# Optimization experiments

Measured on AMD Instinct MI355X. Metric: run time of the kernel, lower is better.

Reference implementation:

```python
import jax, jax.numpy as jnp
import numpy as np

N = 65536    # collocation points
N1 = 1024    # RBF centers
EPS = 0.1    # multiscale parameter used for width init scale


def setup_inputs() -> dict:
    key = jax.random.key(0)
    ks = jax.random.split(key, 10)
    x = jax.random.uniform(ks[0], (N, 2), dtype=jnp.float32)

    def mk(i):
        h = jax.random.uniform(ks[3 * i + 1], (N1,), dtype=jnp.float32)
        c = jax.random.uniform(ks[3 * i + 2], (N1, 2), dtype=jnp.float32)
        w = 5.0 * jax.random.uniform(ks[3 * i + 3], (N1, 2), dtype=jnp.float32) / EPS
        return h, c, w

    h1, c1, w1 = mk(0)
    h2, c2, w2 = mk(1)
    h3, c3, w3 = mk(2)
    return dict(x=x, hight=h1, center=c1, width=w1,
                hight2=h2, center2=c2, width2=w2,
                hight3=h3, center3=c3, width3=w3)


def _rbf(X, c, h, w):
    """Gaussian RBF expansion. X:(N,2) points, c:(N1,2) centers,
    h:(N1,) heights, w:(N1,2) widths. Returns u, du/dx, du/dy, each (N,)."""
    x1 = X[:, 0:1] - c[None, :, 0]          # (N, N1)
    y1 = X[:, 1:2] - c[None, :, 1]          # (N, N1)
    d1 = w[:, 0] ** 2                        # (N1,)
    d2 = w[:, 1] ** 2                        # (N1,)
    e = jnp.exp(-(x1 ** 2) * d1 - (y1 ** 2) * d2)  # (N, N1)
    u = e @ h                                # (N,)
    ux = (-2.0 * x1 * d1 * e) @ h            # (N,)
    uy = (-2.0 * y1 * d2 * e) @ h            # (N,)
    return u, ux, uy


def reference(x, hight, center, width, hight2, center2, width2,
              hight3, center3, width3):
    _, ux, uy = _rbf(x, center, hight, width)
    P, Px, _ = _rbf(x, center2, hight2, width2)
    Q, _, Qy = _rbf(x, center3, hight3, width3)
    return (ux, uy, P, Px, Q, Qy)
```

## Files before the change

kernel.cpp:

```cpp
#include <hip/hip_runtime.h>
#include <math.h>

#define N_PTS  65536
#define N_CTR  1024
#define CHUNK  128
#define PPT    8
#define PPB    (256 * PPT)

#if __has_builtin(__builtin_amdgcn_exp2f)
#define EXP2(x) __builtin_amdgcn_exp2f(x)
#else
#define EXP2(x) exp2f(x)
#endif

__global__ __launch_bounds__(256) void srbf_kernel(
    const float* __restrict__ x,
    const float* __restrict__ h0, const float* __restrict__ c0, const float* __restrict__ w0,
    const float* __restrict__ h1, const float* __restrict__ c1, const float* __restrict__ w1,
    const float* __restrict__ h2, const float* __restrict__ c2, const float* __restrict__ w2,
    float* __restrict__ out)
{
    __shared__ float4 sA[CHUNK];
    __shared__ float4 sB[CHUNK];
    __shared__ float  sC[CHUNK];

    const int bid   = blockIdx.x;
    const int set   = bid >> 8;
    const int r     = bid & 255;
    const int chunk = r >> 5;
    const int pblk  = r & 31;
    const int tid   = threadIdx.x;

    const float*  __restrict__ h = (set == 0) ? h0 : ((set == 1) ? h1 : h2);
    const float2* __restrict__ c = (const float2*)((set == 0) ? c0 : ((set == 1) ? c1 : c2));
    const float2* __restrict__ w = (const float2*)((set == 0) ? w0 : ((set == 1) ? w1 : w2));

    const float LOG2E = 1.4426950408889634f;

    if (tid < CHUNK) {
        const int j = chunk * CHUNK + tid;
        float2 cj = c[j];
        float2 wj = w[j];
        float  hh = h[j];
        float d1 = wj.x * wj.x;
        float d2 = wj.y * wj.y;
        float zb =  2.f * cj.x * d1 * LOG2E;
        float zc = -d1 * LOG2E;
        float zd =  2.f * cj.y * d2 * LOG2E;
        float ze = -d2 * LOG2E;
        float za = -(cj.x * cj.x * d1 + cj.y * cj.y * d2) * LOG2E;
        float k0, k1, k2, k3;
        if (set == 0) {
            k0 = -2.f * hh * d1;
            k1 =  2.f * hh * d1 * cj.x;
            k2 = -2.f * hh * d2;
            k3 =  2.f * hh * d2 * cj.y;
        } else if (set == 1) {
            k0 = hh;
            k1 = -2.f * hh * d1;
            k2 =  2.f * hh * d1 * cj.x;
            k3 = 0.f;
        } else {
            k0 = hh;
            k1 = -2.f * hh * d2;
            k2 =  2.f * hh * d2 * cj.y;
            k3 = 0.f;
        }
        sA[tid] = make_float4(zb, zc, zd, ze);
        sB[tid] = make_float4(za, k0, k1, k2);
        sC[tid] = k3;
    }
    __syncthreads();

    const int base = pblk * PPB + tid;

    float X[PPT], Y[PPT], X2[PPT], Y2[PPT];
    #pragma unroll
    for (int p = 0; p < PPT; ++p) {
        float2 q = ((const float2*)x)[base + p * 256];
        X[p] = q.x;  Y[p] = q.y;
        X2[p] = q.x * q.x;  Y2[p] = q.y * q.y;
    }

    if (set == 0) {
        float A0[PPT], A1[PPT], A2[PPT], A3[PPT];
        #pragma unroll
        for (int p = 0; p < PPT; ++p) { A0[p] = A1[p] = A2[p] = A3[p] = 0.f; }

        #pragma unroll 2
        for (int j = 0; j < CHUNK; ++j) {
            float4 A = sA[j];
            float4 B = sB[j];
            float  k3 = sC[j];
            #pragma unroll
            for (int p = 0; p < PPT; ++p) {
                float s = fmaf(X[p],  A.x, B.x);
                s       = fmaf(X2[p], A.y, s);
                s       = fmaf(Y[p],  A.z, s);
                s       = fmaf(Y2[p], A.w, s);
                float e = EXP2(s);
                A0[p] = fmaf(B.y, e, A0[p]);
                A1[p] = fmaf(B.z, e, A1[p]);
                A2[p] = fmaf(B.w, e, A2[p]);
                A3[p] = fmaf(k3,  e, A3[p]);
            }
        }
        #pragma unroll
        for (int p = 0; p < PPT; ++p) {
            const int i = base + p * 256;
            atomicAdd(&out[i],         fmaf(X[p], A0[p], A1[p]));
            atomicAdd(&out[N_PTS + i], fmaf(Y[p], A2[p], A3[p]));
        }
    } else {
        float A0[PPT], A1[PPT], A2[PPT];
        #pragma unroll
        for (int p = 0; p < PPT; ++p) { A0[p] = A1[p] = A2[p] = 0.f; }

        #pragma unroll 2
        for (int j = 0; j < CHUNK; ++j) {
            float4 A = sA[j];
            float4 B = sB[j];
            #pragma unroll
            for (int p = 0; p < PPT; ++p) {
                float s = fmaf(X[p],  A.x, B.x);
                s       = fmaf(X2[p], A.y, s);
                s       = fmaf(Y[p],  A.z, s);
                s       = fmaf(Y2[p], A.w, s);
                float e = EXP2(s);
                A0[p] = fmaf(B.y, e, A0[p]);
                A1[p] = fmaf(B.z, e, A1[p]);
                A2[p] = fmaf(B.w, e, A2[p]);
            }
        }
        float* o = out + (size_t)set * 2 * N_PTS;
        #pragma unroll
        for (int p = 0; p < PPT; ++p) {
            const int i = base + p * 256;
            const float g = (set == 1) ? X[p] : Y[p];
            atomicAdd(&o[i],         A0[p]);
            atomicAdd(&o[N_PTS + i], fmaf(g, A1[p], A2[p]));
        }
    }
}

extern "C" void kernel_launch(void* const* d_in, const int* in_sizes, int n_in,
                              void* d_out, int out_size, void* d_ws, size_t ws_size,
                              hipStream_t stream) {
    const float* x  = (const float*)d_in[0];
    const float* h1 = (const float*)d_in[1];
    const float* c1 = (const float*)d_in[2];
    const float* w1 = (const float*)d_in[3];
    const float* h2 = (const float*)d_in[4];
    const float* c2 = (const float*)d_in[5];
    const float* w2 = (const float*)d_in[6];
    const float* h3 = (const float*)d_in[7];
    const float* c3 = (const float*)d_in[8];
    const float* w3 = (const float*)d_in[9];

    hipMemsetAsync(d_out, 0, (size_t)out_size * sizeof(float), stream);

    srbf_kernel<<<dim3(768), dim3(256), 0, stream>>>(
        x, h1, c1, w1, h2, c2, w2, h3, c3, w3, (float*)d_out);
}
```

Baseline: 55.21 us.

## Precompute RBF coefficients in a prep kernel and read them uniformly from global memory

Per-center coefficients are now computed once by a separate prep kernel into workspace, instead of each block recomputing them into shared memory behind a barrier. The main kernel drops shared memory and __syncthreads and reads the coefficients with wave-uniform global loads. Chunk size and points per thread are halved, which raises the grid from 768 to 3072 blocks for more parallelism. The costs are an extra kernel launch, twice as many atomic adds to the output, and less reuse of each loaded coefficient across points.

```diff
diff --git a/kernel.cpp b/kernel.cpp
--- a/kernel.cpp
+++ b/kernel.cpp
@@ -3,77 +3,73 @@
 
 #define N_PTS  65536
 #define N_CTR  1024
-#define CHUNK  128
-#define PPT    8
+#define CHUNK  64
+#define PPT    4
 #define PPB    (256 * PPT)
 
 #if __has_builtin(__builtin_amdgcn_exp2f)
-#define EXP2(x) __builtin_amdgcn_exp2f(x)
+#define EXP2(v) __builtin_amdgcn_exp2f(v)
 #else
-#define EXP2(x) exp2f(x)
+#define EXP2(v) exp2f(v)
 #endif
 
-__global__ __launch_bounds__(256) void srbf_kernel(
-    const float* __restrict__ x,
+
+__global__ __launch_bounds__(256) void prep_kernel(
     const float* __restrict__ h0, const float* __restrict__ c0, const float* __restrict__ w0,
     const float* __restrict__ h1, const float* __restrict__ c1, const float* __restrict__ w1,
     const float* __restrict__ h2, const float* __restrict__ c2, const float* __restrict__ w2,
+    float4* __restrict__ RA, float4* __restrict__ RB, float* __restrict__ RC)
+{
+    const int idx = blockIdx.x * 256 + threadIdx.x;
+    if (idx >= 3 * N_CTR) return;
+    const int set = idx >> 10;
+    const int j   = idx & (N_CTR - 1);
+
+    const float*  h = (set == 0) ? h0 : ((set == 1) ? h1 : h2);
+    const float2* c = (const float2*)((set == 0) ? c0 : ((set == 1) ? c1 : c2));
+    const float2* w = (const float2*)((set == 0) ? w0 : ((set == 1) ? w1 : w2));
+
+    const float LOG2E = 1.4426950408889634f;
+    float2 cj = c[j];
+    float2 wj = w[j];
+    float  hh = h[j];
+    float d1 = wj.x * wj.x;
+    float d2 = wj.y * wj.y;
+    float zb =  2.f * cj.x * d1 * LOG2E;
+    float zc = -d1 * LOG2E;
+    float zd =  2.f * cj.y * d2 * LOG2E;
+    float ze = -d2 * LOG2E;
+    float za = -(cj.x * cj.x * d1 + cj.y * cj.y * d2) * LOG2E;
+    float k0, k1, k2, k3;
+    if (set == 0) {
+        k0 = -2.f * hh * d1;  k1 = 2.f * hh * d1 * cj.x;
+        k2 = -2.f * hh * d2;  k3 = 2.f * hh * d2 * cj.y;
+    } else if (set == 1) {
+        k0 = hh;  k1 = -2.f * hh * d1;  k2 = 2.f * hh * d1 * cj.x;  k3 = 0.f;
+    } else {
+        k0 = hh;  k1 = -2.f * hh * d2;  k2 = 2.f * hh * d2 * cj.y;  k3 = 0.f;
+    }
+    RA[idx] = make_float4(zb, zc, zd, ze);
+    RB[idx] = make_float4(za, k0, k1, k2);
+    RC[idx] = k3;
+}
+
+__global__ __launch_bounds__(256) void srbf_main(
+    const float* __restrict__ x,
+    const float4* __restrict__ RA,
+    const float4* __restrict__ RB,
+    const float*  __restrict__ RC,
     float* __restrict__ out)
 {
-    __shared__ float4 sA[CHUNK];
-    __shared__ float4 sB[CHUNK];
-    __shared__ float  sC[CHUNK];
-
     const int bid   = blockIdx.x;
-    const int set   = bid >> 8;
-    const int r     = bid & 255;
-    const int chunk = r >> 5;
-    const int pblk  = r & 31;
+    const int set   = bid >> 10;
+    const int r     = bid & 1023;
+    const int chunk = r >> 6;
+    const int pblk  = r & 63;
     const int tid   = threadIdx.x;
-
-    const float*  __restrict__ h = (set == 0) ? h0 : ((set == 1) ? h1 : h2);
-    const float2* __restrict__ c = (const float2*)((set == 0) ? c0 : ((set == 1) ? c1 : c2));
-    const float2* __restrict__ w = (const float2*)((set == 0) ? w0 : ((set == 1) ? w1 : w2));
-
-    const float LOG2E = 1.4426950408889634f;
-
-    if (tid < CHUNK) {
-        const int j = chunk * CHUNK + tid;
-        float2 cj = c[j];
-        float2 wj = w[j];
-        float  hh = h[j];
-        float d1 = wj.x * wj.x;
-        float d2 = wj.y * wj.y;
-        float zb =  2.f * cj.x * d1 * LOG2E;
-        float zc = -d1 * LOG2E;
-        float zd =  2.f * cj.y * d2 * LOG2E;
-        float ze = -d2 * LOG2E;
-        float za = -(cj.x * cj.x * d1 + cj.y * cj.y * d2) * LOG2E;
-        float k0, k1, k2, k3;
-        if (set == 0) {
-            k0 = -2.f * hh * d1;
-            k1 =  2.f * hh * d1 * cj.x;
-            k2 = -2.f * hh * d2;
-            k3 =  2.f * hh * d2 * cj.y;
-        } else if (set == 1) {
-            k0 = hh;
-            k1 = -2.f * hh * d1;
-            k2 =  2.f * hh * d1 * cj.x;
-            k3 = 0.f;
-        } else {
-            k0 = hh;
-            k1 = -2.f * hh * d2;
-            k2 =  2.f * hh * d2 * cj.y;
-            k3 = 0.f;
-        }
-        sA[tid] = make_float4(zb, zc, zd, ze);
-        sB[tid] = make_float4(za, k0, k1, k2);
-        sC[tid] = k3;
-    }
-    __syncthreads();
+    const int cbase = set * N_CTR + chunk * CHUNK;
 
     const int base = pblk * PPB + tid;
-
     float X[PPT], Y[PPT], X2[PPT], Y2[PPT];
     #pragma unroll
     for (int p = 0; p < PPT; ++p) {
@@ -87,11 +83,11 @@
         #pragma unroll
         for (int p = 0; p < PPT; ++p) { A0[p] = A1[p] = A2[p] = A3[p] = 0.f; }
 
-        #pragma unroll 2
-        for (int j = 0; j < CHUNK; ++j) {
-            float4 A = sA[j];
-            float4 B = sB[j];
-            float  k3 = sC[j];
+        #pragma unroll 4
+        for (int jj = 0; jj < CHUNK; ++jj) {
+            const float4 A = RA[cbase + jj];
+            const float4 B = RB[cbase + jj];
+            const float  k3 = RC[cbase + jj];
             #pragma unroll
             for (int p = 0; p < PPT; ++p) {
                 float s = fmaf(X[p],  A.x, B.x);
@@ -116,10 +112,10 @@
         #pragma unroll
         for (int p = 0; p < PPT; ++p) { A0[p] = A1[p] = A2[p] = 0.f; }
 
-        #pragma unroll 2
-        for (int j = 0; j < CHUNK; ++j) {
-            float4 A = sA[j];
-            float4 B = sB[j];
+        #pragma unroll 4
+        for (int jj = 0; jj < CHUNK; ++jj) {
+            const float4 A = RA[cbase + jj];
+            const float4 B = RB[cbase + jj];
             #pragma unroll
             for (int p = 0; p < PPT; ++p) {
                 float s = fmaf(X[p],  A.x, B.x);
@@ -157,8 +153,15 @@
     const float* c3 = (const float*)d_in[8];
     const float* w3 = (const float*)d_in[9];
 
+    char* ws = (char*)d_ws;
+    float4* RA = (float4*)(ws);
+    float4* RB = (float4*)(ws + 49152);
+    float*  RC = (float*) (ws + 98304);
+
     hipMemsetAsync(d_out, 0, (size_t)out_size * sizeof(float), stream);
 
-    srbf_kernel<<<dim3(768), dim3(256), 0, stream>>>(
-        x, h1, c1, w1, h2, c2, w2, h3, c3, w3, (float*)d_out);
+    prep_kernel<<<dim3(12), dim3(256), 0, stream>>>(
+        h1, c1, w1, h2, c2, w2, h3, c3, w3, RA, RB, RC);
+
+    srbf_main<<<dim3(3072), dim3(256), 0, stream>>>(x, RA, RB, RC, (float*)d_out);
 }
```

After: 59.57 us. 1.08x slower.
